# Performance work log

Hardware: AMD Instinct MI355X
Metric: run time of the kernel (lower is better)

The kernel has to match this reference:

```python
import jax, jax.numpy as jnp
import numpy as np

B, S, H = 2, 2048, 2048
E, K, HID = 8, 2, 4096          # num_experts, top-k, expert hidden (2*H)
NH, HD = 8, 256                  # attention heads, head_dim
MS, MD = 256, 512                # memory_size, memory_dim
RSTEPS, RD = 3, 512              # reasoning steps, reasoning_dim
SCALE = 16.0                     # sqrt(head_dim)


def setup_inputs() -> dict:
    key = jax.random.key(0)
    ks = iter(jax.random.split(key, 64))
    def w(shape, s=0.02):
        return (jax.random.normal(next(ks), shape, jnp.float32) * s)
    z = lambda *shape: jnp.zeros(shape, jnp.float32)
    inp = {
        'hidden_states': jax.random.normal(next(ks), (B, S, H), jnp.float32),
        'attention_mask': jnp.zeros((B, S), jnp.float32),  # 0 = unmasked (faithful: mask*-1e9 added)
        # MoE
        'gate_w': w((H, E)), 'gate_b': z(E),
        'moe_w1': w((E, H, HID)), 'moe_b1': z(E, HID),
        'moe_w2': w((E, HID, H)), 'moe_b2': z(E, H),
        # memory-augmented attention
        'q_w': w((H, H)), 'q_b': z(H),
        'k_w': w((H, H)), 'k_b': z(H),
        'v_w': w((H, H)), 'v_b': z(H),
        'o_w': w((H, H)), 'o_b': z(H),
        'mem_values': jax.random.normal(next(ks), (MS, MD), jnp.float32),
        'mem_proj_w': w((MD, H)), 'mem_proj_b': z(H),
        'mem_attn_w': w((H, MS)), 'mem_attn_b': z(MS),
        # hierarchical reasoning (stacked over steps)
        'rs_w1': w((RSTEPS, H, RD)), 'rs_b1': z(RSTEPS, RD),
        'rs_w2': w((RSTEPS, RD, H)), 'rs_b2': z(RSTEPS, H),
        'ln_g': jnp.ones((RSTEPS, H), jnp.float32), 'ln_b': z(RSTEPS, H),
        'hg_w1': w((RSTEPS, H, H // 4)), 'hg_b1': z(RSTEPS, H // 4),
        'hg_w2': w((RSTEPS, H // 4, 1)), 'hg_b2': z(RSTEPS, 1),
        'integ_w': w((RSTEPS * H, H)), 'integ_b': z(H),
    }
    return inp


def _layernorm(x, g, b, eps=1e-5):
    m = x.mean(-1, keepdims=True)
    v = ((x - m) ** 2).mean(-1, keepdims=True)
    return (x - m) / jnp.sqrt(v + eps) * g + b


def _forward(hidden_states, attention_mask, gate_w, gate_b, moe_w1, moe_b1, moe_w2, moe_b2,
             q_w, q_b, k_w, k_b, v_w, v_b, o_w, o_b, mem_values, mem_proj_w, mem_proj_b,
             mem_attn_w, mem_attn_b, rs_w1, rs_b1, rs_w2, rs_b2, ln_g, ln_b,
             hg_w1, hg_b1, hg_w2, hg_b2, integ_w, integ_b):
    h = hidden_states
    N = B * S
    # ---- Mixture of Experts (top-k routing, dense combine-weight formulation) ----
    x_flat = h.reshape(N, H)
    gate_probs = jax.nn.softmax(x_flat @ gate_w + gate_b, axis=-1)        # [N,E]
    topk_s, topk_i = jax.lax.top_k(gate_probs, K)                          # [N,K]
    topk_p = jax.nn.softmax(topk_s, axis=-1)                               # renormalize over top-k
    comb = jnp.zeros((N, E), x_flat.dtype).at[jnp.arange(N)[:, None], topk_i].add(topk_p)
    h1 = jax.nn.relu(jnp.einsum('nd,edh->neh', x_flat, moe_w1) + moe_b1)   # [N,E,HID]
    eo = jnp.einsum('neh,ehd->ned', h1, moe_w2) + moe_b2                   # [N,E,H]
    moe_out = jnp.einsum('ned,ne->nd', eo, comb).reshape(B, S, H)
    h = h + 0.5 * moe_out
    # ---- Memory-augmented attention ----
    q = (h @ q_w + q_b).reshape(B, S, NH, HD).transpose(0, 2, 1, 3)
    k = (h @ k_w + k_b).reshape(B, S, NH, HD).transpose(0, 2, 1, 3)
    v = (h @ v_w + v_b).reshape(B, S, NH, HD).transpose(0, 2, 1, 3)
    scores = jnp.einsum('bhqd,bhkd->bhqk', q, k) / SCALE
    scores = scores + attention_mask[:, None, None, :] * (-1e9)
    probs = jax.nn.softmax(scores, axis=-1)
    attn = jnp.einsum('bhqk,bhkd->bhqd', probs, v).transpose(0, 2, 1, 3).reshape(B, S, H)
    mem_p = jax.nn.softmax(h @ mem_attn_w + mem_attn_b, axis=-1)           # [B,S,MS]
    mem_o = (mem_p @ mem_values) @ mem_proj_w + mem_proj_b                 # [B,S,H]
    mem_out = (attn + 0.3 * mem_o) @ o_w + o_b
    h = h + mem_out
    # ---- Hierarchical reasoning ----
    cur = h
    outs = []
    for i in range(RSTEPS):
        so = jax.nn.relu(cur @ rs_w1[i] + rs_b1[i]) @ rs_w2[i] + rs_b2[i]
        so = _layernorm(so, ln_g[i], ln_b[i])
        g = jax.nn.sigmoid(jax.nn.relu(cur @ hg_w1[i] + hg_b1[i]) @ hg_w2[i] + hg_b2[i])  # [B,S,1]
        cur = cur + g * so
        outs.append(cur)
    final = jnp.concatenate(outs, axis=-1) @ integ_w + integ_b
    return h + final


def reference(hidden_states, attention_mask, gate_w, gate_b, moe_w1, moe_b1, moe_w2, moe_b2,
              q_w, q_b, k_w, k_b, v_w, v_b, o_w, o_b, mem_values, mem_proj_w, mem_proj_b,
              mem_attn_w, mem_attn_b, rs_w1, rs_b1, rs_w2, rs_b2, ln_g, ln_b,
              hg_w1, hg_b1, hg_w2, hg_b2, integ_w, integ_b):
    return _forward(hidden_states, attention_mask, gate_w, gate_b, moe_w1, moe_b1, moe_w2, moe_b2,
                    q_w, q_b, k_w, k_b, v_w, v_b, o_w, o_b, mem_values, mem_proj_w, mem_proj_b,
                    mem_attn_w, mem_attn_b, rs_w1, rs_b1, rs_w2, rs_b2, ln_g, ln_b,
                    hg_w1, hg_b1, hg_w2, hg_b2, integ_w, integ_b)
```

## Files before the change

### kernel.cpp

```cpp
#include <hip/hip_runtime.h>
#include <string.h>


typedef __attribute__((ext_vector_type(4))) float f32x4;
typedef __attribute__((ext_vector_type(8))) __bf16 bf16x8;

#define NTOK 4096
#define HDIM 2048
#define AS1 __attribute__((address_space(1)))
#define AS3 __attribute__((address_space(3)))

__device__ __forceinline__ unsigned short f2bf(float f) {
  unsigned u = __float_as_uint(f);
  unsigned r = (u + 0x7fffu + ((u >> 16) & 1u)) >> 16;
  return (unsigned short)r;
}
__device__ __forceinline__ float bf2f(unsigned short u) {
  return __uint_as_float(((unsigned)u) << 16);
}
__device__ __forceinline__ void unpack8(uint4 r, float* v) {
  v[0]=bf2f((unsigned short)(r.x&0xffff)); v[1]=bf2f((unsigned short)(r.x>>16));
  v[2]=bf2f((unsigned short)(r.y&0xffff)); v[3]=bf2f((unsigned short)(r.y>>16));
  v[4]=bf2f((unsigned short)(r.z&0xffff)); v[5]=bf2f((unsigned short)(r.z>>16));
  v[6]=bf2f((unsigned short)(r.w&0xffff)); v[7]=bf2f((unsigned short)(r.w>>16));
}
__device__ __forceinline__ uint4 pack8(const float* v) {
  uint4 r;
  r.x = (unsigned)f2bf(v[0]) | ((unsigned)f2bf(v[1])<<16);
  r.y = (unsigned)f2bf(v[2]) | ((unsigned)f2bf(v[3])<<16);
  r.z = (unsigned)f2bf(v[4]) | ((unsigned)f2bf(v[5])<<16);
  r.w = (unsigned)f2bf(v[6]) | ((unsigned)f2bf(v[7])<<16);
  return r;
}

__global__ void k_tconv(const float* __restrict__ in, unsigned short* __restrict__ out,
                        int R, int C, long inB, long outB) {
  __shared__ float tl[32][33];
  const int z = blockIdx.z;
  const float* ip = in + (long)z * inB;
  unsigned short* op = out + (long)z * outB;
  const int tx = threadIdx.x & 31, ty = threadIdx.x >> 5;
  const int c0 = blockIdx.x * 32, r0 = blockIdx.y * 32;
#pragma unroll
  for (int i = 0; i < 4; i++)
    tl[ty + i*8][tx] = ip[(long)(r0 + ty + i*8) * C + c0 + tx];
  __syncthreads();
#pragma unroll
  for (int i = 0; i < 4; i++)
    op[(long)(c0 + ty + i*8) * R + r0 + tx] = f2bf(tl[tx][ty + i*8]);
}

__global__ void k_tconv4(const float* __restrict__ i0, const float* __restrict__ i1,
                         const float* __restrict__ i2, const float* __restrict__ i3,
                         unsigned short* __restrict__ out) {
  __shared__ float tl[32][33];
  const int z = blockIdx.z;
  const float* ip = (z == 0) ? i0 : (z == 1) ? i1 : (z == 2) ? i2 : i3;
  unsigned short* op = out + (size_t)z * 2048 * 2048;
  const int tx = threadIdx.x & 31, ty = threadIdx.x >> 5;
  const int c0 = blockIdx.x * 32, r0 = blockIdx.y * 32;
#pragma unroll
  for (int i = 0; i < 4; i++)
    tl[ty + i*8][tx] = ip[(long)(r0 + ty + i*8) * 2048 + c0 + tx];
  __syncthreads();
#pragma unroll
  for (int i = 0; i < 4; i++)
    op[(long)(c0 + ty + i*8) * 2048 + r0 + tx] = f2bf(tl[tx][ty + i*8]);
}

__global__ void k_tvact(const unsigned short* __restrict__ qkv, unsigned short* __restrict__ vT) {
  __shared__ unsigned short tl[32][33];
  const int z = blockIdx.z, b = z >> 3, hh = z & 7;
  const unsigned short* ip = qkv + (long)b * 2048 * 6144 + 4096 + hh * 256;
  unsigned short* op = vT + (long)z * 256 * 2048;
  const int tx = threadIdx.x & 31, ty = threadIdx.x >> 5;
  const int d0 = blockIdx.x * 32, s0 = blockIdx.y * 32;
#pragma unroll
  for (int i = 0; i < 4; i++)
    tl[ty + i*8][tx] = ip[(long)(s0 + ty + i*8) * 6144 + d0 + tx];
  __syncthreads();
#pragma unroll
  for (int i = 0; i < 4; i++)
    op[(long)(d0 + ty + i*8) * 2048 + s0 + tx] = tl[tx][ty + i*8];
}

__global__ void k_misc(const float* __restrict__ mask, float* __restrict__ mv,
                       const float* __restrict__ qb, const float* __restrict__ kb,
                       const float* __restrict__ vb, float* __restrict__ qkvb,
                       const float* __restrict__ rsb1, const float* __restrict__ hgb1,
                       float* __restrict__ rhb, int* __restrict__ meta) {
  const int b = blockIdx.x, t = threadIdx.x;
  if (b < 16) {
    int i = b * 256 + t; mv[i] = -1e9f * mask[i];
  } else if (b < 40) {
    int i = (b - 16) * 256 + t;
    qkvb[i] = (i < 2048) ? qb[i] : (i < 4096) ? kb[i - 2048] : vb[i - 4096];
  } else if (b < 46) {
    int i = (b - 40) * 256 + t;
    int s = i >> 9, c = i & 511;
    rhb[s * 1024 + c] = rsb1[i]; rhb[s * 1024 + 512 + c] = hgb1[i];
  } else {
    if (t < 8) meta[t] = 0;
  }
}

__global__ void k_gate(const float* __restrict__ x, const float* __restrict__ gw,
                       const float* __restrict__ gb, int* __restrict__ meta,
                       int* __restrict__ e0a, int* __restrict__ e1a,
                       float* __restrict__ w0a, float* __restrict__ w1a,
                       unsigned short* __restrict__ xb) {
  const int wv = threadIdx.x >> 6, ln = threadIdx.x & 63;
  const int n = blockIdx.x * 4 + wv;
  const float* xr = x + (long)n * HDIM;
  unsigned short* xo = xb + (long)n * HDIM;
  float s[8] = {0,0,0,0,0,0,0,0};
  for (int k = ln; k < HDIM; k += 64) {
    float xv = xr[k];
    xo[k] = f2bf(xv);
    const float* g = gw + (long)k * 8;
#pragma unroll
    for (int e = 0; e < 8; e++) s[e] += xv * g[e];
  }
#pragma unroll
  for (int e = 0; e < 8; e++)
    for (int d = 32; d; d >>= 1) s[e] += __shfl_xor(s[e], d);
  if (ln == 0) {
    float mx = -1e30f;
#pragma unroll
    for (int e = 0; e < 8; e++) { s[e] += gb[e]; mx = fmaxf(mx, s[e]); }
    float p[8], sum = 0.f;
#pragma unroll
    for (int e = 0; e < 8; e++) { p[e] = expf(s[e] - mx); sum += p[e]; }
    float inv = 1.f / sum;
#pragma unroll
    for (int e = 0; e < 8; e++) p[e] *= inv;
    int e0 = 0;
    for (int e = 1; e < 8; e++) if (p[e] > p[e0]) e0 = e;
    int e1 = (e0 == 0) ? 1 : 0;
    for (int e = 0; e < 8; e++) if (e != e0 && p[e] > p[e1]) e1 = e;
    float q = expf(p[e1] - p[e0]);
    float w0 = 1.f / (1.f + q), w1 = q / (1.f + q);
    e0a[n] = e0; e1a[n] = e1; w0a[n] = w0; w1a[n] = w1;
    atomicAdd(&meta[e0], 1); atomicAdd(&meta[e1], 1);
  }
}

__global__ void k_buildmap(int* meta) {
  if (threadIdx.x == 0 && blockIdx.x == 0) {
    int cum = 0, nT = 0;
    for (int e = 0; e < 8; e++) {
      int c = meta[e];
      meta[16 + e] = cum; meta[24 + e] = cum + c; meta[8 + e] = 0;
      int t = (c + 127) >> 7;
      for (int i = 0; i < t; i++) { meta[33 + nT] = e; meta[129 + nT] = cum + i * 128; nT++; }
      cum += c;
    }
    meta[32] = nT;
  }
}

__global__ void k_scatter(int* __restrict__ meta, const int* __restrict__ e0a,
                          const int* __restrict__ e1a, int* __restrict__ s0a,
                          int* __restrict__ s1a, int* __restrict__ srcTok) {
  const int n = blockIdx.x * 256 + threadIdx.x;
  if (n < NTOK) {
    int e0 = e0a[n], e1 = e1a[n];
    int s0 = meta[16 + e0] + atomicAdd(&meta[8 + e0], 1);
    int s1 = meta[16 + e1] + atomicAdd(&meta[8 + e1], 1);
    s0a[n] = s0; s1a[n] = s1; srcTok[s0] = n; srcTok[s1] = n;
  }
}

__global__ void k_combine(const float* __restrict__ h, const unsigned short* __restrict__ eo,
                          const int* __restrict__ s0a, const int* __restrict__ s1a,
                          const float* __restrict__ w0a, const float* __restrict__ w1a,
                          unsigned short* __restrict__ h2b) {
  const int n = blockIdx.x, c = threadIdx.x * 8;
  const float w0 = w0a[n], w1 = w1a[n];
  uint4 a = *(const uint4*)(eo + (long)s0a[n] * HDIM + c);
  uint4 b = *(const uint4*)(eo + (long)s1a[n] * HDIM + c);
  float va[8], vb[8]; unpack8(a, va); unpack8(b, vb);
  const float* hr = h + (long)n * HDIM + c;
  float o[8];
#pragma unroll
  for (int j = 0; j < 8; j++) o[j] = hr[j] + 0.5f * (w0 * va[j] + w1 * vb[j]);
  *(uint4*)(h2b + (long)n * HDIM + c) = pack8(o);
}

__global__ void k_softmax256(const float* __restrict__ in, unsigned short* __restrict__ out) {
  const int wv = threadIdx.x >> 6, ln = threadIdx.x & 63;
  const long r = (long)blockIdx.x * 4 + wv;
  const float4 v4 = ((const float4*)(in + r * 256))[ln];
  float v[4] = {v4.x, v4.y, v4.z, v4.w};
  float m = fmaxf(fmaxf(v[0], v[1]), fmaxf(v[2], v[3]));
  for (int d = 32; d; d >>= 1) m = fmaxf(m, __shfl_xor(m, d));
  float s = 0.f;
#pragma unroll
  for (int j = 0; j < 4; j++) { v[j] = expf(v[j] - m); s += v[j]; }
  for (int d = 32; d; d >>= 1) s += __shfl_xor(s, d);
  const float inv = 1.f / s;
  union { unsigned short u[4]; uint2 d2; } p;
#pragma unroll
  for (int j = 0; j < 4; j++) p.u[j] = f2bf(v[j] * inv);
  ((uint2*)(out + r * 256))[ln] = p.d2;
}

__global__ void k_gdot(const unsigned short* __restrict__ g1, long ld, const float* __restrict__ w,
                       const float* __restrict__ bb, float* __restrict__ gv) {
  const int wv = threadIdx.x >> 6, ln = threadIdx.x & 63;
  const int n = blockIdx.x * 4 + wv;
  uint4 raw = *(const uint4*)(g1 + (long)n * ld + ln * 8);
  float v[8]; unpack8(raw, v);
  const float4 wa = ((const float4*)w)[ln * 2];
  const float4 wb = ((const float4*)w)[ln * 2 + 1];
  float s = v[0]*wa.x + v[1]*wa.y + v[2]*wa.z + v[3]*wa.w
          + v[4]*wb.x + v[5]*wb.y + v[6]*wb.z + v[7]*wb.w;
  for (int d = 32; d; d >>= 1) s += __shfl_xor(s, d);
  if (ln == 0) gv[n] = 1.f / (1.f + expf(-(s + bb[0])));
}

__global__ void k_lnupdate(const unsigned short* __restrict__ so,
                           const unsigned short* __restrict__ curIn,
                           const float* __restrict__ gv, const float* __restrict__ lng,
                           const float* __restrict__ lnb,
                           unsigned short* __restrict__ curbOut,
                           unsigned short* __restrict__ outs, int step) {
  const int n = blockIdx.x, t = threadIdx.x, wv = t >> 6, ln = t & 63, c = t * 8;
  uint4 raw = *(const uint4*)(so + (long)n * 2048 + c);
  float x[8]; unpack8(raw, x);
  float s1 = 0.f, s2 = 0.f;
#pragma unroll
  for (int j = 0; j < 8; j++) { s1 += x[j]; s2 += x[j] * x[j]; }
  for (int d = 32; d; d >>= 1) { s1 += __shfl_xor(s1, d); s2 += __shfl_xor(s2, d); }
  __shared__ float a1[4], a2[4];
  if (ln == 0) { a1[wv] = s1; a2[wv] = s2; }
  __syncthreads();
  s1 = a1[0] + a1[1] + a1[2] + a1[3];
  s2 = a2[0] + a2[1] + a2[2] + a2[3];
  const float mean = s1 * (1.f / 2048.f);
  const float var = s2 * (1.f / 2048.f) - mean * mean;
  const float rstd = rsqrtf(var + 1e-5f);
  const float g = gv[n];
  uint4 ci = *(const uint4*)(curIn + (long)n * 2048 + c);
  float cv[8]; unpack8(ci, cv);
  float o[8];
#pragma unroll
  for (int j = 0; j < 8; j++) {
    float l = (x[j] - mean) * rstd * lng[c + j] + lnb[c + j];
    o[j] = cv[j] + g * l;
  }
  const uint4 pk = pack8(o);
  *(uint4*)(curbOut + (long)n * 2048 + c) = pk;
  *(uint4*)(outs + (long)n * 6144 + (long)step * 2048 + c) = pk;
}

struct GArgs {
  const unsigned short* A; long lda, aSO, aSI;
  const unsigned short* Bt; long ldb, bSO, bSI;
  int M, N, K;
  const float* adv; long advSO, advSI;
  float alpha, rscale;
  const float* rF; long ldrF, rfSO, rfSI;
  const unsigned short* rB; long ldrB, rbSO, rbSI;
  float* oF; long ldoF, ofSO, ofSI;
  unsigned short* oB; long ldoB, obSO, obSI;
  const int* meta;
  const int* srcTok;
};

template <int MOE, int RELU, int RESID, int OUTF, int OUTB>
__global__ __launch_bounds__(512) void gemm_bt(GArgs g) {
  __shared__ unsigned short lds[2 * 16384];
  const int t = threadIdx.x, wv = t >> 6, ln = t & 63, ln15 = ln & 15;
  const int lr8 = ln >> 3;
  const int lsl = (ln & 7) ^ lr8;
  const int bz = blockIdx.z;
  int row0, rowMax;
  const unsigned short *A, *Bt;
  long advO = 0, rFO = 0, rBO = 0, oFO = 0, oBO = 0;
  if constexpr (MOE) {
    const int ty = blockIdx.y;
    if (ty >= g.meta[32]) return;
    const int e = g.meta[33 + ty];
    row0 = g.meta[129 + ty]; rowMax = g.meta[24 + e];
    A = g.A; Bt = g.Bt + (long)e * g.bSO;
    advO = (long)e * g.advSO;
  } else {
    row0 = blockIdx.y << 7; rowMax = g.M;
    const long bo = (long)(bz >> 3), bi = (long)(bz & 7);
    A = g.A + bo * g.aSO + bi * g.aSI;
    Bt = g.Bt + bo * g.bSO + bi * g.bSI;
    advO = bo * g.advSO + bi * g.advSI;
    rFO = bo * g.rfSO + bi * g.rfSI;
    rBO = bo * g.rbSO + bi * g.rbSI;
    oFO = bo * g.ofSO + bi * g.ofSI;
    oBO = bo * g.obSO + bi * g.obSI;
  }
  const int col0 = blockIdx.x << 7;
  const long lda = g.lda, ldb = g.ldb;
  const int wm = (wv >> 2) << 6;
  const int wc = (wv & 3) << 5;

  int grow0, grow1;
  {
    int r0i = row0 + (wv << 4) + lr8;
    int r1i = r0i + 8;
    if constexpr (MOE) {
      r0i = (r0i < rowMax) ? r0i : (rowMax - 1);
      r1i = (r1i < rowMax) ? r1i : (rowMax - 1);
    }
    if constexpr (MOE == 2) { grow0 = g.srcTok[r0i]; grow1 = g.srcTok[r1i]; }
    else { grow0 = r0i; grow1 = r1i; }
  }

  auto STAGE = [&](int kt, unsigned base) {
    const long kk = ((long)kt << 6) + (lsl << 3);
    {
      const int rb = (wv << 4);
      __builtin_amdgcn_global_load_lds(
          (const AS1 void*)(A + (long)grow0 * lda + kk),
          (AS3 void*)(lds + base + (rb << 6)), 16, 0, 0);
      __builtin_amdgcn_global_load_lds(
          (const AS1 void*)(A + (long)grow1 * lda + kk),
          (AS3 void*)(lds + base + ((rb + 8) << 6)), 16, 0, 0);
    }
#pragma unroll
    for (int l = 0; l < 2; ++l) {
      const int rb = (wv << 4) + (l << 3);
      __builtin_amdgcn_global_load_lds(
          (const AS1 void*)(Bt + (long)(col0 + rb + lr8) * ldb + kk),
          (AS3 void*)(lds + base + 8192 + (rb << 6)), 16, 0, 0);
    }
  };

  const f32x4 fz = {0.f, 0.f, 0.f, 0.f};
  f32x4 acc[4][2];
#pragma unroll
  for (int i = 0; i < 4; i++)
#pragma unroll
    for (int j = 0; j < 2; j++) acc[i][j] = fz;

  const int nt = g.K >> 6;

  STAGE(0, 0);
  asm volatile("s_waitcnt vmcnt(0)" ::: "memory");
  __builtin_amdgcn_s_barrier();

  for (int kt = 0; kt < nt; ++kt) {
    const unsigned aB = (kt & 1) ? 16384u : 0u;
    const unsigned nB = aB ^ 16384u;
    if (kt + 1 < nt) STAGE(kt + 1, nB);
#pragma unroll
    for (int ks = 0; ks < 2; ++ks) {
      const int kb = (ks << 2) + (ln >> 4);
      bf16x8 bg[2];
#pragma unroll
      for (int j = 0; j < 2; ++j) {
        const int r = wc + (j << 4) + ln15;
        bg[j] = *(const bf16x8*)(lds + aB + 8192 + (r << 6) + ((kb ^ (r & 7)) << 3));
      }
      __builtin_amdgcn_s_setprio(1);
#pragma unroll
      for (int i = 0; i < 4; ++i) {
        const int r = wm + (i << 4) + ln15;
        bf16x8 a = *(const bf16x8*)(lds + aB + (r << 6) + ((kb ^ (r & 7)) << 3));
#pragma unroll
        for (int j = 0; j < 2; ++j)
          acc[i][j] = __builtin_amdgcn_mfma_f32_16x16x32_bf16(a, bg[j], acc[i][j], 0, 0, 0);
      }
      __builtin_amdgcn_s_setprio(0);
    }
    asm volatile("s_waitcnt vmcnt(0)" ::: "memory");
    __builtin_amdgcn_s_barrier();
  }

#pragma unroll
  for (int i = 0; i < 4; i++) {
#pragma unroll
    for (int j = 0; j < 2; j++) {
      const int cc = col0 + wc + (j << 4) + ln15;
      const float av = g.adv ? g.adv[advO + cc] : 0.f;
#pragma unroll
      for (int r = 0; r < 4; r++) {
        const int rr = row0 + wm + (i << 4) + ((ln >> 4) << 2) + r;
        if (rr < rowMax) {
          float v = g.alpha * acc[i][j][r] + av;
          if constexpr (RELU) v = fmaxf(v, 0.f);
          if constexpr (RESID == 1) v = g.rF[rFO + (long)rr * g.ldrF + cc] + g.rscale * v;
          if constexpr (RESID == 2) v = bf2f(g.rB[rBO + (long)rr * g.ldrB + cc]) + g.rscale * v;
          if constexpr (OUTF) g.oF[oFO + (long)rr * g.ldoF + cc] = v;
          if constexpr (OUTB) g.oB[oBO + (long)rr * g.ldoB + cc] = f2bf(v);
        }
      }
    }
  }
}

__global__ __launch_bounds__(512) void k_pv(const unsigned short* __restrict__ S,
                                            const unsigned short* __restrict__ Vt,
                                            unsigned short* __restrict__ O) {
  __shared__ unsigned short lds[4096 + 16384];
  __shared__ float pm[64][8], ps[64][8];
  __shared__ float smax[64], sinv[64];
  const int t = threadIdx.x, wv = t >> 6, ln = t & 63, ln15 = ln & 15;
  const int lr8 = ln >> 3, lk = ln & 7;
  const int lsl = lk ^ lr8;
  const int rt = blockIdx.x, bh = blockIdx.y;
  const int b = bh >> 3, hh = bh & 7;
  const int row0 = rt << 6;
  const unsigned short* Sb = S + (long)bh * 2048 * 2048;
  const unsigned short* Vb = Vt + (long)bh * 256 * 2048;

  {
    const int r = t >> 3, sg = t & 7;
    const unsigned short* p = Sb + (long)(row0 + r) * 2048 + sg * 256;
    float m = -3.0e38f, s = 0.f;
    for (int i = 0; i < 32; ++i) {
      uint4 raw = ((const uint4*)p)[i];
      float v[8]; unpack8(raw, v);
      float m8 = v[0];
#pragma unroll
      for (int j = 1; j < 8; j++) m8 = fmaxf(m8, v[j]);
      const float mn = fmaxf(m, m8);
      s *= expf(m - mn);
#pragma unroll
      for (int j = 0; j < 8; j++) s += expf(v[j] - mn);
      m = mn;
    }
    pm[r][sg] = m; ps[r][sg] = s;
  }
  __syncthreads();
  if (t < 64) {
    float m = pm[t][0];
#pragma unroll
    for (int j = 1; j < 8; j++) m = fmaxf(m, pm[t][j]);
    float s = 0.f;
#pragma unroll
    for (int j = 0; j < 8; j++) s += ps[t][j] * expf(pm[t][j] - m);
    smax[t] = m; sinv[t] = 1.f / s;
  }
  __syncthreads();
  const int arow = (wv << 3) + lr8;
  const float am = smax[arow], ainv = sinv[arow];

  const f32x4 fz = {0.f, 0.f, 0.f, 0.f};
  f32x4 acc[4][2];
#pragma unroll
  for (int i = 0; i < 4; i++)
#pragma unroll
    for (int j = 0; j < 2; j++) acc[i][j] = fz;

  const int wc = wv << 5;

  for (int kt = 0; kt < 32; ++kt) {
    const long kk = ((long)kt << 6) + (lsl << 3);
    const uint4 araw = *(const uint4*)(Sb + (long)(row0 + arow) * 2048 + kk);
#pragma unroll
    for (int l = 0; l < 4; ++l) {
      const int rb = (l << 6) + (wv << 3);
      __builtin_amdgcn_global_load_lds(
          (const AS1 void*)(Vb + (long)(rb + lr8) * 2048 + kk),
          (AS3 void*)(lds + 4096 + (rb << 6)), 16, 0, 0);
    }
    {
      float v[8]; unpack8(araw, v);
      float pvv[8];
#pragma unroll
      for (int j = 0; j < 8; j++) pvv[j] = expf(v[j] - am) * ainv;
      *(uint4*)(lds + (arow << 6) + (lk << 3)) = pack8(pvv);
    }
    __syncthreads();
#pragma unroll
    for (int ks = 0; ks < 2; ++ks) {
      const int kb = (ks << 2) + (ln >> 4);
      bf16x8 bg[2];
#pragma unroll
      for (int j = 0; j < 2; ++j) {
        const int r = wc + (j << 4) + ln15;
        bg[j] = *(const bf16x8*)(lds + 4096 + (r << 6) + ((kb ^ (r & 7)) << 3));
      }
      __builtin_amdgcn_s_setprio(1);
#pragma unroll
      for (int i = 0; i < 4; ++i) {
        const int r = (i << 4) + ln15;
        bf16x8 a = *(const bf16x8*)(lds + (r << 6) + ((kb ^ (r & 7)) << 3));
#pragma unroll
        for (int j = 0; j < 2; ++j)
          acc[i][j] = __builtin_amdgcn_mfma_f32_16x16x32_bf16(a, bg[j], acc[i][j], 0, 0, 0);
      }
      __builtin_amdgcn_s_setprio(0);
    }
    __syncthreads();
  }

  unsigned short* Ob = O + (long)b * 2048 * 2048 + hh * 256;
#pragma unroll
  for (int i = 0; i < 4; ++i) {
#pragma unroll
    for (int j = 0; j < 2; ++j) {
      const int cc = wc + (j << 4) + ln15;
#pragma unroll
      for (int r = 0; r < 4; ++r) {
        const int rr = row0 + (i << 4) + ((ln >> 4) << 2) + r;
        Ob[(long)rr * 2048 + cc] = f2bf(acc[i][j][r]);
      }
    }
  }
}

static constexpr size_t O_W1T = 0;
static constexpr size_t O_W2T = O_W1T + (size_t)8 * 4096 * 2048 * 2;
static constexpr size_t O_QT  = O_W2T + (size_t)8 * 4096 * 2048 * 2;
static constexpr size_t O_MAT = O_QT + (size_t)4 * 2048 * 2048 * 2;
static constexpr size_t O_MPT = O_MAT + (size_t)256 * 2048 * 2;
static constexpr size_t O_MVT = O_MPT + (size_t)2048 * 512 * 2;
static constexpr size_t O_RH1 = O_MVT + (size_t)512 * 256 * 2;
static constexpr size_t O_RS2 = O_RH1 + (size_t)3 * 1024 * 2048 * 2;
static constexpr size_t O_IGT = O_RS2 + (size_t)3 * 2048 * 512 * 2;
static constexpr size_t O_META= O_IGT + (size_t)2048 * 6144 * 2;
static constexpr size_t O_E0  = O_META + 4096;
static constexpr size_t O_E1  = O_E0 + 16384;
static constexpr size_t O_W0  = O_E1 + 16384;
static constexpr size_t O_W1  = O_W0 + 16384;
static constexpr size_t O_S0  = O_W1 + 16384;
static constexpr size_t O_S1  = O_S0 + 16384;
static constexpr size_t O_SRC = O_S1 + 16384;
static constexpr size_t O_MSK = O_SRC + 32768;
static constexpr size_t O_GV  = O_MSK + 16384;
static constexpr size_t O_QKVB= O_GV + 16384;
static constexpr size_t O_RHB = O_QKVB + 6144 * 4;
static constexpr size_t O_H2B = O_RHB + 3072 * 4;
static constexpr size_t O_H3B = O_H2B + (size_t)4096 * 2048 * 2;
static constexpr size_t O_ATT = O_H3B + (size_t)4096 * 2048 * 2;
static constexpr size_t O_AO2 = O_ATT + (size_t)4096 * 2048 * 2;
static constexpr size_t O_MLG = O_AO2 + (size_t)4096 * 2048 * 2;
static constexpr size_t O_MPB = O_MLG + (size_t)4096 * 256 * 4;
static constexpr size_t O_MPV = O_MPB + (size_t)4096 * 256 * 2;
static constexpr size_t O_AR  = O_MPV + (size_t)4096 * 512 * 2;
static constexpr size_t O_XB = O_AR;
static constexpr size_t O_H1 = O_XB + (size_t)4096 * 2048 * 2 + (size_t)8192 * 2048 * 2;
static constexpr size_t O_EO = O_H1 + (size_t)8192 * 4096 * 2;
static constexpr size_t O_QB = O_XB + (size_t)4096 * 2048 * 2;
static constexpr size_t O_VT = O_QB + (size_t)3 * 4096 * 2048 * 2;
static constexpr size_t O_SC = O_VT + (size_t)4096 * 2048 * 2;
static constexpr size_t O_T1 = O_QB;
static constexpr size_t O_SOB= O_T1 + (size_t)4096 * 1024 * 2;
static constexpr size_t O_CRB= O_SOB + (size_t)4096 * 2048 * 2;
static constexpr size_t O_OUS= O_CRB + (size_t)4096 * 2048 * 2;

extern "C" void kernel_launch(void* const* d_in, const int* in_sizes, int n_in,
                              void* d_out, int out_size, void* d_ws, size_t ws_size,
                              hipStream_t stream) {
  (void)in_sizes; (void)n_in; (void)out_size; (void)ws_size;
  const float* h        = (const float*)d_in[0];
  const float* mask     = (const float*)d_in[1];
  const float* gate_w   = (const float*)d_in[2];
  const float* gate_b   = (const float*)d_in[3];
  const float* moe_w1   = (const float*)d_in[4];
  const float* moe_b1   = (const float*)d_in[5];
  const float* moe_w2   = (const float*)d_in[6];
  const float* moe_b2   = (const float*)d_in[7];
  const float* q_w      = (const float*)d_in[8];
  const float* q_b      = (const float*)d_in[9];
  const float* k_w      = (const float*)d_in[10];
  const float* k_b      = (const float*)d_in[11];
  const float* v_w      = (const float*)d_in[12];
  const float* v_b      = (const float*)d_in[13];
  const float* o_w      = (const float*)d_in[14];
  const float* o_b      = (const float*)d_in[15];
  const float* mem_vals = (const float*)d_in[16];
  const float* mproj_w  = (const float*)d_in[17];
  const float* mproj_b  = (const float*)d_in[18];
  const float* mattn_w  = (const float*)d_in[19];
  const float* mattn_b  = (const float*)d_in[20];
  const float* rs_w1    = (const float*)d_in[21];
  const float* rs_b1    = (const float*)d_in[22];
  const float* rs_w2    = (const float*)d_in[23];
  const float* rs_b2    = (const float*)d_in[24];
  const float* ln_g     = (const float*)d_in[25];
  const float* ln_b     = (const float*)d_in[26];
  const float* hg_w1    = (const float*)d_in[27];
  const float* hg_b1    = (const float*)d_in[28];
  const float* hg_w2    = (const float*)d_in[29];
  const float* hg_b2    = (const float*)d_in[30];
  const float* integ_w  = (const float*)d_in[31];
  const float* integ_b  = (const float*)d_in[32];

  char* ws = (char*)d_ws;
  auto U = [&](size_t o) { return (unsigned short*)(ws + o); };
  auto F = [&](size_t o) { return (float*)(ws + o); };
  auto I = [&](size_t o) { return (int*)(ws + o); };

  k_tconv<<<dim3(128, 64, 8), 256, 0, stream>>>(moe_w1, U(O_W1T), 2048, 4096, 8388608, 8388608);
  k_tconv<<<dim3(64, 128, 8), 256, 0, stream>>>(moe_w2, U(O_W2T), 4096, 2048, 8388608, 8388608);
  k_tconv4<<<dim3(64, 64, 4), 256, 0, stream>>>(q_w, k_w, v_w, o_w, U(O_QT));
  k_tconv<<<dim3(8, 64, 1), 256, 0, stream>>>(mattn_w, U(O_MAT), 2048, 256, 0, 0);
  k_tconv<<<dim3(64, 16, 1), 256, 0, stream>>>(mproj_w, U(O_MPT), 512, 2048, 0, 0);
  k_tconv<<<dim3(16, 8, 1), 256, 0, stream>>>(mem_vals, U(O_MVT), 256, 512, 0, 0);
  k_tconv<<<dim3(16, 64, 3), 256, 0, stream>>>(rs_w1, U(O_RH1), 2048, 512, 2048 * 512, 1024 * 2048);
  k_tconv<<<dim3(16, 64, 3), 256, 0, stream>>>(hg_w1, U(O_RH1) + (size_t)512 * 2048, 2048, 512,
                                               2048 * 512, 1024 * 2048);
  k_tconv<<<dim3(64, 16, 3), 256, 0, stream>>>(rs_w2, U(O_RS2), 512, 2048, 512 * 2048, 512 * 2048);
  k_tconv<<<dim3(64, 192, 1), 256, 0, stream>>>(integ_w, U(O_IGT), 6144, 2048, 0, 0);
  k_misc<<<47, 256, 0, stream>>>(mask, F(O_MSK), q_b, k_b, v_b, F(O_QKVB),
                                 rs_b1, hg_b1, F(O_RHB), I(O_META));

  k_gate<<<1024, 256, 0, stream>>>(h, gate_w, gate_b, I(O_META), I(O_E0), I(O_E1),
                                   F(O_W0), F(O_W1), U(O_XB));
  k_buildmap<<<1, 1, 0, stream>>>(I(O_META));
  k_scatter<<<16, 256, 0, stream>>>(I(O_META), I(O_E0), I(O_E1), I(O_S0), I(O_S1), I(O_SRC));

  GArgs z0; memset(&z0, 0, sizeof(z0)); z0.alpha = 1.f; z0.rscale = 1.f;
  {
    GArgs g = z0;
    g.A = U(O_XB); g.lda = 2048;
    g.Bt = U(O_W1T); g.ldb = 2048; g.bSO = (long)4096 * 2048;
    g.N = 4096; g.K = 2048;
    g.adv = moe_b1; g.advSO = 4096;
    g.oB = U(O_H1); g.ldoB = 4096;
    g.meta = I(O_META); g.srcTok = I(O_SRC);
    gemm_bt<2, 1, 0, 0, 1><<<dim3(32, 72, 1), 512, 0, stream>>>(g);
  }
  {
    GArgs g = z0;
    g.A = U(O_H1); g.lda = 4096;
    g.Bt = U(O_W2T); g.ldb = 4096; g.bSO = (long)2048 * 4096;
    g.N = 2048; g.K = 4096;
    g.adv = moe_b2; g.advSO = 2048;
    g.oB = U(O_EO); g.ldoB = 2048;
    g.meta = I(O_META);
    gemm_bt<1, 0, 0, 0, 1><<<dim3(16, 72, 1), 512, 0, stream>>>(g);
  }
  k_combine<<<4096, 256, 0, stream>>>(h, U(O_EO), I(O_S0), I(O_S1), F(O_W0), F(O_W1), U(O_H2B));

  {
    GArgs g = z0;
    g.A = U(O_H2B); g.lda = 2048; g.M = 4096; g.N = 6144; g.K = 2048;
    g.Bt = U(O_QT); g.ldb = 2048;
    g.adv = F(O_QKVB);
    g.oB = U(O_QB); g.ldoB = 6144;
    gemm_bt<0, 0, 0, 0, 1><<<dim3(48, 32, 1), 512, 0, stream>>>(g);
  }
  k_tvact<<<dim3(8, 64, 16), 256, 0, stream>>>(U(O_QB), U(O_VT));
  {
    GArgs g = z0;
    g.A = U(O_QB); g.lda = 6144; g.aSO = 12582912; g.aSI = 256;
    g.Bt = U(O_QB) + 2048; g.ldb = 6144; g.bSO = 12582912; g.bSI = 256;
    g.M = 2048; g.N = 2048; g.K = 256;
    g.adv = F(O_MSK); g.advSO = 2048; g.advSI = 0;
    g.alpha = 0.0625f;
    g.oB = U(O_SC); g.ldoB = 2048; g.obSO = 33554432; g.obSI = 4194304;
    gemm_bt<0, 0, 0, 0, 1><<<dim3(16, 16, 16), 512, 0, stream>>>(g);
  }
  k_pv<<<dim3(32, 16, 1), 512, 0, stream>>>(U(O_SC), U(O_VT), U(O_ATT));
  {
    GArgs g = z0;
    g.A = U(O_H2B); g.lda = 2048; g.Bt = U(O_MAT); g.ldb = 2048;
    g.M = 4096; g.N = 256; g.K = 2048;
    g.adv = mattn_b;
    g.oF = F(O_MLG); g.ldoF = 256;
    gemm_bt<0, 0, 0, 1, 0><<<dim3(2, 32, 1), 512, 0, stream>>>(g);
  }
  k_softmax256<<<1024, 256, 0, stream>>>(F(O_MLG), U(O_MPB));
  {
    GArgs g = z0;
    g.A = U(O_MPB); g.lda = 256; g.Bt = U(O_MVT); g.ldb = 256;
    g.M = 4096; g.N = 512; g.K = 256;
    g.oB = U(O_MPV); g.ldoB = 512;
    gemm_bt<0, 0, 0, 0, 1><<<dim3(4, 32, 1), 512, 0, stream>>>(g);
  }
  {
    GArgs g = z0;
    g.A = U(O_MPV); g.lda = 512; g.Bt = U(O_MPT); g.ldb = 512;
    g.M = 4096; g.N = 2048; g.K = 512;
    g.adv = mproj_b;
    g.rB = U(O_ATT); g.ldrB = 2048; g.rscale = 0.3f;
    g.oB = U(O_AO2); g.ldoB = 2048;
    gemm_bt<0, 0, 2, 0, 1><<<dim3(16, 32, 1), 512, 0, stream>>>(g);
  }
  {
    GArgs g = z0;
    g.A = U(O_AO2); g.lda = 2048; g.Bt = U(O_QT) + (size_t)3 * 2048 * 2048; g.ldb = 2048;
    g.M = 4096; g.N = 2048; g.K = 2048;
    g.adv = o_b;
    g.rB = U(O_H2B); g.ldrB = 2048; g.rscale = 1.f;
    g.oB = U(O_H3B); g.ldoB = 2048;
    gemm_bt<0, 0, 2, 0, 1><<<dim3(16, 32, 1), 512, 0, stream>>>(g);
  }

  for (int i = 0; i < 3; i++) {
    const unsigned short* curb = (i == 0) ? U(O_H3B) : U(O_CRB);
    {
      GArgs g = z0;
      g.A = curb; g.lda = 2048;
      g.Bt = U(O_RH1) + (size_t)i * 1024 * 2048; g.ldb = 2048;
      g.M = 4096; g.N = 1024; g.K = 2048;
      g.adv = F(O_RHB) + i * 1024;
      g.oB = U(O_T1); g.ldoB = 1024;
      gemm_bt<0, 1, 0, 0, 1><<<dim3(8, 32, 1), 512, 0, stream>>>(g);
    }
    {
      GArgs g = z0;
      g.A = U(O_T1); g.lda = 1024;
      g.Bt = U(O_RS2) + (size_t)i * 2048 * 512; g.ldb = 512;
      g.M = 4096; g.N = 2048; g.K = 512;
      g.adv = rs_b2 + i * 2048;
      g.oB = U(O_SOB); g.ldoB = 2048;
      gemm_bt<0, 0, 0, 0, 1><<<dim3(16, 32, 1), 512, 0, stream>>>(g);
    }
    k_gdot<<<1024, 256, 0, stream>>>(U(O_T1) + 512, 1024, hg_w2 + i * 512, hg_b2 + i, F(O_GV));
    k_lnupdate<<<4096, 256, 0, stream>>>(U(O_SOB), curb, F(O_GV), ln_g + i * 2048,
                                         ln_b + i * 2048, U(O_CRB), U(O_OUS), i);
  }
  {
    GArgs g = z0;
    g.A = U(O_OUS); g.lda = 6144; g.Bt = U(O_IGT); g.ldb = 6144;
    g.M = 4096; g.N = 2048; g.K = 6144;
    g.adv = integ_b;
    g.rB = U(O_H3B); g.ldrB = 2048; g.rscale = 1.f;
    g.oF = (float*)d_out; g.ldoF = 2048;
    gemm_bt<0, 0, 2, 1, 0><<<dim3(16, 32, 1), 512, 0, stream>>>(g);
  }
}
```

Baseline: 1.592 ms.

## Fuse memory-attention logits into QKV GEMM and compute softmax stats in score epilogue

The memory-attention logit projection is appended as 256 extra output columns of the QKV GEMM, so a separate GEMM launch and its fp32 logits buffer go away, and the memory softmax now reads bf16 logits. The score GEMM also gains an epilogue that computes per-row, per-tile max and sum-exp partials and writes them to a stats buffer. The PV kernel then merges these 16 partials instead of re-reading the full bf16 score matrix to find row max and sum. The trade-off is lower-precision memory logits and extra epilogue work and register pressure in the score GEMM.

```diff
diff --git a/kernel.cpp b/kernel.cpp
--- a/kernel.cpp
+++ b/kernel.cpp
@@ -56,7 +56,7 @@
   __shared__ float tl[32][33];
   const int z = blockIdx.z;
   const float* ip = (z == 0) ? i0 : (z == 1) ? i1 : (z == 2) ? i2 : i3;
-  unsigned short* op = out + (size_t)z * 2048 * 2048;
+  unsigned short* op = out + ((z < 3) ? (size_t)z * 2048 * 2048 : (size_t)6400 * 2048);
   const int tx = threadIdx.x & 31, ty = threadIdx.x >> 5;
   const int c0 = blockIdx.x * 32, r0 = blockIdx.y * 32;
 #pragma unroll
@@ -71,13 +71,13 @@
 __global__ void k_tvact(const unsigned short* __restrict__ qkv, unsigned short* __restrict__ vT) {
   __shared__ unsigned short tl[32][33];
   const int z = blockIdx.z, b = z >> 3, hh = z & 7;
-  const unsigned short* ip = qkv + (long)b * 2048 * 6144 + 4096 + hh * 256;
+  const unsigned short* ip = qkv + (long)b * 2048 * 6400 + 4096 + hh * 256;
   unsigned short* op = vT + (long)z * 256 * 2048;
   const int tx = threadIdx.x & 31, ty = threadIdx.x >> 5;
   const int d0 = blockIdx.x * 32, s0 = blockIdx.y * 32;
 #pragma unroll
   for (int i = 0; i < 4; i++)
-    tl[ty + i*8][tx] = ip[(long)(s0 + ty + i*8) * 6144 + d0 + tx];
+    tl[ty + i*8][tx] = ip[(long)(s0 + ty + i*8) * 6400 + d0 + tx];
   __syncthreads();
 #pragma unroll
   for (int i = 0; i < 4; i++)
@@ -86,17 +86,20 @@
 
 __global__ void k_misc(const float* __restrict__ mask, float* __restrict__ mv,
                        const float* __restrict__ qb, const float* __restrict__ kb,
-                       const float* __restrict__ vb, float* __restrict__ qkvb,
+                       const float* __restrict__ vb, const float* __restrict__ mb,
+                       float* __restrict__ qkvb,
                        const float* __restrict__ rsb1, const float* __restrict__ hgb1,
                        float* __restrict__ rhb, int* __restrict__ meta) {
   const int b = blockIdx.x, t = threadIdx.x;
   if (b < 16) {
     int i = b * 256 + t; mv[i] = -1e9f * mask[i];
-  } else if (b < 40) {
+  } else if (b < 41) {
     int i = (b - 16) * 256 + t;
-    qkvb[i] = (i < 2048) ? qb[i] : (i < 4096) ? kb[i - 2048] : vb[i - 4096];
-  } else if (b < 46) {
-    int i = (b - 40) * 256 + t;
+    if (i < 6400)
+      qkvb[i] = (i < 2048) ? qb[i] : (i < 4096) ? kb[i - 2048]
+              : (i < 6144) ? vb[i - 4096] : mb[i - 6144];
+  } else if (b < 47) {
+    int i = (b - 41) * 256 + t;
     int s = i >> 9, c = i & 511;
     rhb[s * 1024 + c] = rsb1[i]; rhb[s * 1024 + 512 + c] = hgb1[i];
   } else {
@@ -187,11 +190,14 @@
   *(uint4*)(h2b + (long)n * HDIM + c) = pack8(o);
 }
 
-__global__ void k_softmax256(const float* __restrict__ in, unsigned short* __restrict__ out) {
+__global__ void k_softmax256(const unsigned short* __restrict__ in, long ld,
+                             unsigned short* __restrict__ out) {
   const int wv = threadIdx.x >> 6, ln = threadIdx.x & 63;
   const long r = (long)blockIdx.x * 4 + wv;
-  const float4 v4 = ((const float4*)(in + r * 256))[ln];
-  float v[4] = {v4.x, v4.y, v4.z, v4.w};
+  uint2 raw = ((const uint2*)(in + r * ld))[ln];
+  float v[4];
+  v[0]=bf2f((unsigned short)(raw.x&0xffff)); v[1]=bf2f((unsigned short)(raw.x>>16));
+  v[2]=bf2f((unsigned short)(raw.y&0xffff)); v[3]=bf2f((unsigned short)(raw.y>>16));
   float m = fmaxf(fmaxf(v[0], v[1]), fmaxf(v[2], v[3]));
   for (int d = 32; d; d >>= 1) m = fmaxf(m, __shfl_xor(m, d));
   float s = 0.f;
@@ -266,9 +272,10 @@
   unsigned short* oB; long ldoB, obSO, obSI;
   const int* meta;
   const int* srcTok;
+  float* stat;
 };
 
-template <int MOE, int RELU, int RESID, int OUTF, int OUTB>
+template <int MOE, int RELU, int RESID, int OUTF, int OUTB, int STAT = 0>
 __global__ __launch_bounds__(512) void gemm_bt(GArgs g) {
   __shared__ unsigned short lds[2 * 16384];
   const int t = threadIdx.x, wv = t >> 6, ln = t & 63, ln15 = ln & 15;
@@ -374,6 +381,7 @@
     __builtin_amdgcn_s_barrier();
   }
 
+  float vv[4][2][4];
 #pragma unroll
   for (int i = 0; i < 4; i++) {
 #pragma unroll
@@ -388,19 +396,59 @@
           if constexpr (RELU) v = fmaxf(v, 0.f);
           if constexpr (RESID == 1) v = g.rF[rFO + (long)rr * g.ldrF + cc] + g.rscale * v;
           if constexpr (RESID == 2) v = bf2f(g.rB[rBO + (long)rr * g.ldrB + cc]) + g.rscale * v;
+          if constexpr (STAT) vv[i][j][r] = v;
           if constexpr (OUTF) g.oF[oFO + (long)rr * g.ldoF + cc] = v;
           if constexpr (OUTB) g.oB[oBO + (long)rr * g.ldoB + cc] = f2bf(v);
+        } else if constexpr (STAT) {
+          vv[i][j][r] = -3.0e38f;
         }
       }
     }
   }
+  if constexpr (STAT) {
+    float* stm = (float*)lds;
+    float* sts = stm + 512;
+#pragma unroll
+    for (int i = 0; i < 4; i++) {
+#pragma unroll
+      for (int r = 0; r < 4; r++) {
+        float m = fmaxf(vv[i][0][r], vv[i][1][r]);
+        float s = expf(vv[i][0][r] - m) + expf(vv[i][1][r] - m);
+#pragma unroll
+        for (int d = 1; d < 16; d <<= 1) {
+          float m2 = __shfl_xor(m, d), s2 = __shfl_xor(s, d);
+          float mn = fmaxf(m, m2);
+          s = s * expf(m - mn) + s2 * expf(m2 - mn);
+          m = mn;
+        }
+        if (ln15 == 0) {
+          const int row = wm + (i << 4) + ((ln >> 4) << 2) + r;
+          stm[row * 4 + (wv & 3)] = m;
+          sts[row * 4 + (wv & 3)] = s;
+        }
+      }
+    }
+    __syncthreads();
+    if (t < 128) {
+      float m = stm[t * 4], s = sts[t * 4];
+#pragma unroll
+      for (int q = 1; q < 4; q++) {
+        float m2 = stm[t * 4 + q], s2 = sts[t * 4 + q];
+        float mn = fmaxf(m, m2);
+        s = s * expf(m - mn) + s2 * expf(m2 - mn);
+        m = mn;
+      }
+      float2 o; o.x = m; o.y = s;
+      ((float2*)g.stat)[((long)bz * 2048 + row0 + t) * 16 + blockIdx.x] = o;
+    }
+  }
 }
 
 __global__ __launch_bounds__(512) void k_pv(const unsigned short* __restrict__ S,
                                             const unsigned short* __restrict__ Vt,
+                                            const float2* __restrict__ sst,
                                             unsigned short* __restrict__ O) {
   __shared__ unsigned short lds[4096 + 16384];
-  __shared__ float pm[64][8], ps[64][8];
   __shared__ float smax[64], sinv[64];
   const int t = threadIdx.x, wv = t >> 6, ln = t & 63, ln15 = ln & 15;
   const int lr8 = ln >> 3, lk = ln & 7;
@@ -411,32 +459,16 @@
   const unsigned short* Sb = S + (long)bh * 2048 * 2048;
   const unsigned short* Vb = Vt + (long)bh * 256 * 2048;
 
-  {
-    const int r = t >> 3, sg = t & 7;
-    const unsigned short* p = Sb + (long)(row0 + r) * 2048 + sg * 256;
-    float m = -3.0e38f, s = 0.f;
-    for (int i = 0; i < 32; ++i) {
-      uint4 raw = ((const uint4*)p)[i];
-      float v[8]; unpack8(raw, v);
-      float m8 = v[0];
-#pragma unroll
-      for (int j = 1; j < 8; j++) m8 = fmaxf(m8, v[j]);
-      const float mn = fmaxf(m, m8);
-      s *= expf(m - mn);
-#pragma unroll
-      for (int j = 0; j < 8; j++) s += expf(v[j] - mn);
+  if (t < 64) {
+    const float2* st = sst + ((long)bh * 2048 + row0 + t) * 16;
+    float m = st[0].x, s = st[0].y;
+#pragma unroll
+    for (int q = 1; q < 16; q++) {
+      float2 p = st[q];
+      float mn = fmaxf(m, p.x);
+      s = s * expf(m - mn) + p.y * expf(p.x - mn);
       m = mn;
     }
-    pm[r][sg] = m; ps[r][sg] = s;
-  }
-  __syncthreads();
-  if (t < 64) {
-    float m = pm[t][0];
-#pragma unroll
-    for (int j = 1; j < 8; j++) m = fmaxf(m, pm[t][j]);
-    float s = 0.f;
-#pragma unroll
-    for (int j = 0; j < 8; j++) s += ps[t][j] * expf(pm[t][j] - m);
     smax[t] = m; sinv[t] = 1.f / s;
   }
   __syncthreads();
@@ -511,8 +543,8 @@
 static constexpr size_t O_W1T = 0;
 static constexpr size_t O_W2T = O_W1T + (size_t)8 * 4096 * 2048 * 2;
 static constexpr size_t O_QT  = O_W2T + (size_t)8 * 4096 * 2048 * 2;
-static constexpr size_t O_MAT = O_QT + (size_t)4 * 2048 * 2048 * 2;
-static constexpr size_t O_MPT = O_MAT + (size_t)256 * 2048 * 2;
+static constexpr size_t O_OT  = O_QT + (size_t)6400 * 2048 * 2;
+static constexpr size_t O_MPT = O_QT + (size_t)8448 * 2048 * 2;
 static constexpr size_t O_MVT = O_MPT + (size_t)2048 * 512 * 2;
 static constexpr size_t O_RH1 = O_MVT + (size_t)512 * 256 * 2;
 static constexpr size_t O_RS2 = O_RH1 + (size_t)3 * 1024 * 2048 * 2;
@@ -528,20 +560,20 @@
 static constexpr size_t O_MSK = O_SRC + 32768;
 static constexpr size_t O_GV  = O_MSK + 16384;
 static constexpr size_t O_QKVB= O_GV + 16384;
-static constexpr size_t O_RHB = O_QKVB + 6144 * 4;
+static constexpr size_t O_RHB = O_QKVB + 6400 * 4;
 static constexpr size_t O_H2B = O_RHB + 3072 * 4;
 static constexpr size_t O_H3B = O_H2B + (size_t)4096 * 2048 * 2;
 static constexpr size_t O_ATT = O_H3B + (size_t)4096 * 2048 * 2;
 static constexpr size_t O_AO2 = O_ATT + (size_t)4096 * 2048 * 2;
-static constexpr size_t O_MLG = O_AO2 + (size_t)4096 * 2048 * 2;
-static constexpr size_t O_MPB = O_MLG + (size_t)4096 * 256 * 4;
+static constexpr size_t O_SST = O_AO2 + (size_t)4096 * 2048 * 2;
+static constexpr size_t O_MPB = O_SST + (size_t)16 * 2048 * 16 * 8;
 static constexpr size_t O_MPV = O_MPB + (size_t)4096 * 256 * 2;
 static constexpr size_t O_AR  = O_MPV + (size_t)4096 * 512 * 2;
 static constexpr size_t O_XB = O_AR;
 static constexpr size_t O_H1 = O_XB + (size_t)4096 * 2048 * 2 + (size_t)8192 * 2048 * 2;
 static constexpr size_t O_EO = O_H1 + (size_t)8192 * 4096 * 2;
 static constexpr size_t O_QB = O_XB + (size_t)4096 * 2048 * 2;
-static constexpr size_t O_VT = O_QB + (size_t)3 * 4096 * 2048 * 2;
+static constexpr size_t O_VT = O_QB + (size_t)4096 * 6400 * 2;
 static constexpr size_t O_SC = O_VT + (size_t)4096 * 2048 * 2;
 static constexpr size_t O_T1 = O_QB;
 static constexpr size_t O_SOB= O_T1 + (size_t)4096 * 1024 * 2;
@@ -594,7 +626,7 @@
   k_tconv<<<dim3(128, 64, 8), 256, 0, stream>>>(moe_w1, U(O_W1T), 2048, 4096, 8388608, 8388608);
   k_tconv<<<dim3(64, 128, 8), 256, 0, stream>>>(moe_w2, U(O_W2T), 4096, 2048, 8388608, 8388608);
   k_tconv4<<<dim3(64, 64, 4), 256, 0, stream>>>(q_w, k_w, v_w, o_w, U(O_QT));
-  k_tconv<<<dim3(8, 64, 1), 256, 0, stream>>>(mattn_w, U(O_MAT), 2048, 256, 0, 0);
+  k_tconv<<<dim3(8, 64, 1), 256, 0, stream>>>(mattn_w, U(O_QT) + (size_t)6144 * 2048, 2048, 256, 0, 0);
   k_tconv<<<dim3(64, 16, 1), 256, 0, stream>>>(mproj_w, U(O_MPT), 512, 2048, 0, 0);
   k_tconv<<<dim3(16, 8, 1), 256, 0, stream>>>(mem_vals, U(O_MVT), 256, 512, 0, 0);
   k_tconv<<<dim3(16, 64, 3), 256, 0, stream>>>(rs_w1, U(O_RH1), 2048, 512, 2048 * 512, 1024 * 2048);
@@ -602,7 +634,7 @@
                                                2048 * 512, 1024 * 2048);
   k_tconv<<<dim3(64, 16, 3), 256, 0, stream>>>(rs_w2, U(O_RS2), 512, 2048, 512 * 2048, 512 * 2048);
   k_tconv<<<dim3(64, 192, 1), 256, 0, stream>>>(integ_w, U(O_IGT), 6144, 2048, 0, 0);
-  k_misc<<<47, 256, 0, stream>>>(mask, F(O_MSK), q_b, k_b, v_b, F(O_QKVB),
+  k_misc<<<48, 256, 0, stream>>>(mask, F(O_MSK), q_b, k_b, v_b, mattn_b, F(O_QKVB),
                                  rs_b1, hg_b1, F(O_RHB), I(O_META));
 
   k_gate<<<1024, 256, 0, stream>>>(h, gate_w, gate_b, I(O_META), I(O_E0), I(O_E1),
@@ -635,33 +667,26 @@
 
   {
     GArgs g = z0;
-    g.A = U(O_H2B); g.lda = 2048; g.M = 4096; g.N = 6144; g.K = 2048;
+    g.A = U(O_H2B); g.lda = 2048; g.M = 4096; g.N = 6400; g.K = 2048;
     g.Bt = U(O_QT); g.ldb = 2048;
     g.adv = F(O_QKVB);
-    g.oB = U(O_QB); g.ldoB = 6144;
-    gemm_bt<0, 0, 0, 0, 1><<<dim3(48, 32, 1), 512, 0, stream>>>(g);
+    g.oB = U(O_QB); g.ldoB = 6400;
+    gemm_bt<0, 0, 0, 0, 1><<<dim3(50, 32, 1), 512, 0, stream>>>(g);
   }
   k_tvact<<<dim3(8, 64, 16), 256, 0, stream>>>(U(O_QB), U(O_VT));
   {
     GArgs g = z0;
-    g.A = U(O_QB); g.lda = 6144; g.aSO = 12582912; g.aSI = 256;
-    g.Bt = U(O_QB) + 2048; g.ldb = 6144; g.bSO = 12582912; g.bSI = 256;
+    g.A = U(O_QB); g.lda = 6400; g.aSO = (long)2048 * 6400; g.aSI = 256;
+    g.Bt = U(O_QB) + 2048; g.ldb = 6400; g.bSO = (long)2048 * 6400; g.bSI = 256;
     g.M = 2048; g.N = 2048; g.K = 256;
     g.adv = F(O_MSK); g.advSO = 2048; g.advSI = 0;
     g.alpha = 0.0625f;
     g.oB = U(O_SC); g.ldoB = 2048; g.obSO = 33554432; g.obSI = 4194304;
-    gemm_bt<0, 0, 0, 0, 1><<<dim3(16, 16, 16), 512, 0, stream>>>(g);
-  }
-  k_pv<<<dim3(32, 16, 1), 512, 0, stream>>>(U(O_SC), U(O_VT), U(O_ATT));
-  {
-    GArgs g = z0;
-    g.A = U(O_H2B); g.lda = 2048; g.Bt = U(O_MAT); g.ldb = 2048;
-    g.M = 4096; g.N = 256; g.K = 2048;
-    g.adv = mattn_b;
-    g.oF = F(O_MLG); g.ldoF = 256;
-    gemm_bt<0, 0, 0, 1, 0><<<dim3(2, 32, 1), 512, 0, stream>>>(g);
-  }
-  k_softmax256<<<1024, 256, 0, stream>>>(F(O_MLG), U(O_MPB));
+    g.stat = F(O_SST);
+    gemm_bt<0, 0, 0, 0, 1, 1><<<dim3(16, 16, 16), 512, 0, stream>>>(g);
+  }
+  k_pv<<<dim3(32, 16, 1), 512, 0, stream>>>(U(O_SC), U(O_VT), (const float2*)F(O_SST), U(O_ATT));
+  k_softmax256<<<1024, 256, 0, stream>>>(U(O_QB) + 6144, 6400, U(O_MPB));
   {
     GArgs g = z0;
     g.A = U(O_MPB); g.lda = 256; g.Bt = U(O_MVT); g.ldb = 256;
@@ -680,7 +705,7 @@
   }
   {
     GArgs g = z0;
-    g.A = U(O_AO2); g.lda = 2048; g.Bt = U(O_QT) + (size_t)3 * 2048 * 2048; g.ldb = 2048;
+    g.A = U(O_AO2); g.lda = 2048; g.Bt = U(O_OT); g.ldb = 2048;
     g.M = 4096; g.N = 2048; g.K = 2048;
     g.adv = o_b;
     g.rB = U(O_H2B); g.ldrB = 2048; g.rscale = 1.f;
```

Measured after the change: 1.714 ms. +7.6%, slower.
